# Performance work log

Hardware: AMD Instinct MI355X
Metric: run time of the kernel (lower is better)

## Reference

```python
import jax, jax.numpy as jnp
import numpy as np

IN_F = 4096
OUT_F = 4096
RANK = 16
N_BITS = 4
ALPHA = 1.0
GROUP = 128
Q_N = -(2 ** (N_BITS - 1))       # -8 for 4-bit signed
Q_P = 2 ** (N_BITS - 1) - 1      # +7
EPS = 1e-9


def setup_inputs() -> dict:
    key = jax.random.key(0)
    k0, k1, k2, k3, k4, k5 = jax.random.split(key, 6)
    x = jax.random.normal(k0, (8, 1024, IN_F), dtype=jnp.float32)
    w0 = jax.random.normal(k1, (OUT_F, IN_F), dtype=jnp.float32) * 0.02
    lora_a = jax.random.normal(k2, (RANK, IN_F), dtype=jnp.float32) * 0.02
    lora_b = jax.random.normal(k3, (OUT_F, RANK), dtype=jnp.float32) * 0.02
    num_groups = (OUT_F * IN_F) // GROUP
    q_scale = jnp.abs(jax.random.normal(k4, (num_groups,), dtype=jnp.float32)) * 0.01 + 0.005
    bias = jax.random.normal(k5, (OUT_F,), dtype=jnp.float32) * 0.01
    return {"x": x, "w0": w0, "lora_a": lora_a, "lora_b": lora_b,
            "q_scale": q_scale, "bias": bias}


def _quantize_weight(w0, lora_a, lora_b, q_scale):
    # LoRA merge: w_comb = w0 + alpha * (B @ A)   -> (OUT_F, IN_F)
    w_comb = w0 + ALPHA * (lora_b @ lora_a)
    num_groups = w_comb.size // GROUP
    w_g = w_comb.reshape(num_groups, GROUP)          # grouped view
    s = q_scale[:, None]                             # (G, 1) per-group scale
    w_scaled = w_g / (s + EPS)
    clamped = jnp.clip(w_scaled, Q_N, Q_P)
    q_int = jnp.round(clamped)
    w_q = (q_int * s).reshape(w_comb.shape)          # dequantized fake-quant weight
    return w_q


def reference(x, w0, lora_a, lora_b, q_scale, bias):
    w_q = _quantize_weight(w0, lora_a, lora_b, q_scale)
    # F.linear(x, w_q) + bias : (B, S, IN) @ (IN, OUT)
    return jnp.einsum('bsi,oi->bso', x, w_q) + bias
```

## Files before the change

kernel.cpp:

```cpp
#include <hip/hip_runtime.h>
#include <hip/hip_bf16.h>
#include <stdint.h>
#include <stddef.h>

#define IN_F   4096
#define OUT_F  4096
#define RANK   16
#define GROUP  128
#define M_TOT  8192

#define BM     256
#define BN     256
#define BK     32
#define NIT    (IN_F / BK)
#define HALF_B 16384
#define TILE_B 32768
#define LDS_B  (3 * TILE_B)

typedef __bf16 bf16_t;
typedef __bf16 bf16x4 __attribute__((ext_vector_type(4)));
typedef __bf16 bf16x8 __attribute__((ext_vector_type(8)));
typedef float  f32x4  __attribute__((ext_vector_type(4)));

__device__ static inline void load_lds16(const void* g, void* l) {
  __builtin_amdgcn_global_load_lds(
      (const __attribute__((address_space(1))) unsigned int*)g,
      (__attribute__((address_space(3))) unsigned int*)l,
      16, 0, 0);
}

__global__ void __launch_bounds__(256)
quant_kernel(const float* __restrict__ w0, const float* __restrict__ la,
             const float* __restrict__ lb, const float* __restrict__ qs,
             bf16_t* __restrict__ wq)
{
  const int o = blockIdx.y;
  const int i = blockIdx.x * 1024 + threadIdx.x * 4;

  __shared__ float lbr[RANK];
  if (threadIdx.x < RANK) lbr[threadIdx.x] = lb[o * RANK + threadIdx.x];
  __syncthreads();

  const size_t off = (size_t)o * IN_F + i;
  const float4 w = *(const float4*)(w0 + off);
  float a0 = w.x, a1 = w.y, a2 = w.z, a3 = w.w;
  #pragma unroll
  for (int r = 0; r < RANK; ++r) {
    const float4 av = *(const float4*)(la + (size_t)r * IN_F + i);
    const float bv = lbr[r];
    a0 = fmaf(bv, av.x, a0);
    a1 = fmaf(bv, av.y, a1);
    a2 = fmaf(bv, av.z, a2);
    a3 = fmaf(bv, av.w, a3);
  }
  const float s   = qs[o * (IN_F / GROUP) + (i >> 7)];
  const float inv = 1.0f / (s + 1e-9f);
  const float q0 = rintf(fminf(fmaxf(a0 * inv, -8.0f), 7.0f)) * s;
  const float q1 = rintf(fminf(fmaxf(a1 * inv, -8.0f), 7.0f)) * s;
  const float q2 = rintf(fminf(fmaxf(a2 * inv, -8.0f), 7.0f)) * s;
  const float q3 = rintf(fminf(fmaxf(a3 * inv, -8.0f), 7.0f)) * s;
  bf16x4 v;
  v[0] = (bf16_t)q0; v[1] = (bf16_t)q1; v[2] = (bf16_t)q2; v[3] = (bf16_t)q3;
  *(bf16x4*)(wq + off) = v;
}

__global__ void __launch_bounds__(256)
castx_kernel(const float* __restrict__ x, bf16_t* __restrict__ xb)
{
  const size_t i = ((size_t)blockIdx.x * 256 + threadIdx.x) * 8;
  const float4 a = *(const float4*)(x + i);
  const float4 b = *(const float4*)(x + i + 4);
  bf16x8 v;
  v[0] = (bf16_t)a.x; v[1] = (bf16_t)a.y; v[2] = (bf16_t)a.z; v[3] = (bf16_t)a.w;
  v[4] = (bf16_t)b.x; v[5] = (bf16_t)b.y; v[6] = (bf16_t)b.z; v[7] = (bf16_t)b.w;
  *(bf16x8*)(xb + i) = v;
}

__global__ void __launch_bounds__(512, 2)
gemm_kernel(const bf16_t* __restrict__ A, const bf16_t* __restrict__ Bw,
            const float* __restrict__ bias, float* __restrict__ C)
{
  extern __shared__ __align__(16) char smem[];

  const int tid  = threadIdx.x;
  const int lane = tid & 63;
  const int lr   = lane & 15;
  const int quad = lane >> 4;
  const int wid  = tid >> 6;
  const int wm   = wid >> 2;
  const int wn   = wid & 3;

  const int bid = blockIdx.x;
  const int swz = (bid & 7) * 64 + (bid >> 3);
  const int m0  = (swz >> 4) * BM;
  const int n0  = (swz & 15) * BN;

  const int srow = tid >> 2;
  const int scol = ((tid & 3) ^ ((tid >> 3) & 3)) * 8;
  const bf16_t* gA0 = A  + (size_t)(m0 + srow) * IN_F + scol;
  const bf16_t* gA1 = gA0 + (size_t)128 * IN_F;
  const bf16_t* gB0 = Bw + (size_t)(n0 + srow) * IN_F + scol;
  const bf16_t* gB1 = gB0 + (size_t)128 * IN_F;

  const int rswz = (quad ^ ((lr >> 1) & 3)) * 16;
  const int aOff = (wm * 128 + lr) * 64 + rswz;
  const int bOff = (wn * 64  + lr) * 64 + rswz;

  f32x4 acc[8][4];
  #pragma unroll
  for (int i = 0; i < 8; ++i)
    #pragma unroll
    for (int j = 0; j < 4; ++j)
      acc[i][j] = (f32x4){0.f, 0.f, 0.f, 0.f};

  bf16x8 bfr0[4], bfr1[4], afA[4], afB[4];

  auto stageA = [&](int T, char* buf) {
    const size_t ko = (size_t)T * BK;
    load_lds16(gA0 + ko, buf + tid * 16);
    load_lds16(gA1 + ko, buf + tid * 16 + 8192);
  };
  auto stageB = [&](int T, char* buf) {
    const size_t ko = (size_t)T * BK;
    load_lds16(gB0 + ko, buf + HALF_B + tid * 16);
    load_lds16(gB1 + ko, buf + HALF_B + tid * 16 + 8192);
  };

  auto ph_even = [&](int T, const char* rbuf, char* wbuf, bf16x8 (&bcur)[4]) {
    __builtin_amdgcn_s_barrier();
    __builtin_amdgcn_sched_barrier(0);
    if (T + 2 < NIT) stageA(T + 2, wbuf);
    #pragma unroll
    for (int f = 0; f < 4; ++f)
      afB[f] = *(const bf16x8*)(rbuf + aOff + 4096 + f * 1024);
    __builtin_amdgcn_sched_barrier(0);
    __builtin_amdgcn_s_setprio(1);
    #pragma unroll
    for (int fm = 0; fm < 4; ++fm)
      #pragma unroll
      for (int fn = 0; fn < 4; ++fn)
        acc[fm][fn] = __builtin_amdgcn_mfma_f32_16x16x32_bf16(
            afA[fm], bcur[fn], acc[fm][fn], 0, 0, 0);
    __builtin_amdgcn_s_setprio(0);
  };

  auto ph_odd = [&](int T, const char* rnext, char* wbuf,
                    bf16x8 (&bcur)[4], bf16x8 (&bnxt)[4]) {
    if (T + 2 < NIT) asm volatile("s_waitcnt vmcnt(2)" ::: "memory");
    else             asm volatile("s_waitcnt vmcnt(0)" ::: "memory");
    __builtin_amdgcn_s_barrier();
    __builtin_amdgcn_sched_barrier(0);
    if (T + 2 < NIT) stageB(T + 2, wbuf);
    if (T + 1 < NIT) {
      #pragma unroll
      for (int f = 0; f < 4; ++f)
        bnxt[f] = *(const bf16x8*)(rnext + HALF_B + bOff + f * 1024);
      #pragma unroll
      for (int f = 0; f < 4; ++f)
        afA[f] = *(const bf16x8*)(rnext + aOff + f * 1024);
    }
    __builtin_amdgcn_sched_barrier(0);
    __builtin_amdgcn_s_setprio(1);
    #pragma unroll
    for (int fm = 0; fm < 4; ++fm)
      #pragma unroll
      for (int fn = 0; fn < 4; ++fn)
        acc[4 + fm][fn] = __builtin_amdgcn_mfma_f32_16x16x32_bf16(
            afB[fm], bcur[fn], acc[4 + fm][fn], 0, 0, 0);
    __builtin_amdgcn_s_setprio(0);
  };

  {
    stageA(0, smem);          stageB(0, smem);
    stageA(1, smem + TILE_B); stageB(1, smem + TILE_B);
    asm volatile("s_waitcnt vmcnt(4)" ::: "memory");
    __builtin_amdgcn_s_barrier();
    __builtin_amdgcn_sched_barrier(0);
    #pragma unroll
    for (int f = 0; f < 4; ++f)
      bfr0[f] = *(const bf16x8*)(smem + HALF_B + bOff + f * 1024);
    #pragma unroll
    for (int f = 0; f < 4; ++f)
      afA[f] = *(const bf16x8*)(smem + aOff + f * 1024);
  }

  int rb = 0;
  for (int tt = 0; tt < NIT; tt += 2) {
    const int rb1 = (rb + 1 == 3) ? 0 : rb + 1;
    const int rb2 = (rb1 + 1 == 3) ? 0 : rb1 + 1;
    char* b_rb  = smem + rb  * TILE_B;
    char* b_rb1 = smem + rb1 * TILE_B;
    char* b_rb2 = smem + rb2 * TILE_B;

    ph_even(tt,     b_rb,  b_rb2, bfr0);
    ph_odd (tt,     b_rb1, b_rb2, bfr0, bfr1);
    ph_even(tt + 1, b_rb1, b_rb,  bfr1);
    ph_odd (tt + 1, b_rb2, b_rb,  bfr1, bfr0);

    rb = rb2;
  }

  #pragma unroll
  for (int fn = 0; fn < 4; ++fn) {
    const int gn = n0 + wn * 64 + fn * 16 + lr;
    const float bv = bias[gn];
    #pragma unroll
    for (int fm = 0; fm < 8; ++fm) {
      const int gm = m0 + wm * 128 + fm * 16 + quad * 4;
      #pragma unroll
      for (int r = 0; r < 4; ++r)
        C[(size_t)(gm + r) * OUT_F + gn] = acc[fm][fn][r] + bv;
    }
  }
}

extern "C" void kernel_launch(void* const* d_in, const int* in_sizes, int n_in,
                              void* d_out, int out_size, void* d_ws, size_t ws_size,
                              hipStream_t stream) {
  const float* x    = (const float*)d_in[0];
  const float* w0   = (const float*)d_in[1];
  const float* la   = (const float*)d_in[2];
  const float* lb   = (const float*)d_in[3];
  const float* qs   = (const float*)d_in[4];
  const float* bias = (const float*)d_in[5];
  float* out = (float*)d_out;

  bf16_t* wq = (bf16_t*)d_ws;
  bf16_t* xb = (bf16_t*)((char*)d_ws + (size_t)OUT_F * IN_F * 2);

  static bool attr_done = false;
  if (!attr_done) {
    (void)hipFuncSetAttribute((const void*)gemm_kernel,
                              hipFuncAttributeMaxDynamicSharedMemorySize,
                              LDS_B);
    attr_done = true;
  }

  quant_kernel<<<dim3(IN_F / 1024, OUT_F), 256, 0, stream>>>(w0, la, lb, qs, wq);
  castx_kernel<<<(M_TOT * IN_F) / (256 * 8), 256, 0, stream>>>(x, xb);
  gemm_kernel<<<dim3((M_TOT / BM) * (OUT_F / BN)), 512, LDS_B, stream>>>(
      xb, wq, bias, out);
}
```

Measured before the change: 544.2 us.

## Merge global-to-LDS stages into one barrier phase and interleave with MFMAs

Removes the barrier and the A-tile stage from the even phase. Both A and B next-tile loads are now issued in the odd phase after a full vmcnt(0) wait, so each K-step has one barrier instead of two. sched_group_barrier hints interleave the MFMAs with the LDS reads and VMEM issues, aiming to hide latency under matrix work. The trade-off is that waiting on all outstanding loads before the barrier shortens prefetch distance and may expose global memory latency.

New measurement: 560.2 us. 1.03x slower.

```diff
diff --git a/kernel.cpp b/kernel.cpp
--- a/kernel.cpp
+++ b/kernel.cpp
@@ -126,31 +126,34 @@
     load_lds16(gB1 + ko, buf + HALF_B + tid * 16 + 8192);
   };
 
-  auto ph_even = [&](int T, const char* rbuf, char* wbuf, bf16x8 (&bcur)[4]) {
-    __builtin_amdgcn_s_barrier();
-    __builtin_amdgcn_sched_barrier(0);
-    if (T + 2 < NIT) stageA(T + 2, wbuf);
+  auto ph_even = [&](int T, const char* rbuf, bf16x8 (&bcur)[4]) {
+    __builtin_amdgcn_s_setprio(1);
     #pragma unroll
     for (int f = 0; f < 4; ++f)
       afB[f] = *(const bf16x8*)(rbuf + aOff + 4096 + f * 1024);
-    __builtin_amdgcn_sched_barrier(0);
-    __builtin_amdgcn_s_setprio(1);
     #pragma unroll
     for (int fm = 0; fm < 4; ++fm)
       #pragma unroll
       for (int fn = 0; fn < 4; ++fn)
         acc[fm][fn] = __builtin_amdgcn_mfma_f32_16x16x32_bf16(
             afA[fm], bcur[fn], acc[fm][fn], 0, 0, 0);
+    #pragma unroll
+    for (int g = 0; g < 4; ++g) {
+      __builtin_amdgcn_sched_group_barrier(0x008, 2, 0);
+      __builtin_amdgcn_sched_group_barrier(0x100, 1, 0);
+    }
+    __builtin_amdgcn_sched_group_barrier(0x008, 8, 0);
     __builtin_amdgcn_s_setprio(0);
+    __builtin_amdgcn_sched_barrier(0);
   };
 
   auto ph_odd = [&](int T, const char* rnext, char* wbuf,
                     bf16x8 (&bcur)[4], bf16x8 (&bnxt)[4]) {
-    if (T + 2 < NIT) asm volatile("s_waitcnt vmcnt(2)" ::: "memory");
-    else             asm volatile("s_waitcnt vmcnt(0)" ::: "memory");
+    asm volatile("s_waitcnt vmcnt(0)" ::: "memory");
     __builtin_amdgcn_s_barrier();
     __builtin_amdgcn_sched_barrier(0);
-    if (T + 2 < NIT) stageB(T + 2, wbuf);
+    __builtin_amdgcn_s_setprio(1);
+    if (T + 2 < NIT) { stageA(T + 2, wbuf); stageB(T + 2, wbuf); }
     if (T + 1 < NIT) {
       #pragma unroll
       for (int f = 0; f < 4; ++f)
@@ -159,15 +162,25 @@
       for (int f = 0; f < 4; ++f)
         afA[f] = *(const bf16x8*)(rnext + aOff + f * 1024);
     }
-    __builtin_amdgcn_sched_barrier(0);
-    __builtin_amdgcn_s_setprio(1);
     #pragma unroll
     for (int fm = 0; fm < 4; ++fm)
       #pragma unroll
       for (int fn = 0; fn < 4; ++fn)
         acc[4 + fm][fn] = __builtin_amdgcn_mfma_f32_16x16x32_bf16(
             afB[fm], bcur[fn], acc[4 + fm][fn], 0, 0, 0);
+    #pragma unroll
+    for (int g = 0; g < 4; ++g) {
+      __builtin_amdgcn_sched_group_barrier(0x008, 1, 0);
+      __builtin_amdgcn_sched_group_barrier(0x010, 1, 0);
+    }
+    #pragma unroll
+    for (int g = 0; g < 8; ++g) {
+      __builtin_amdgcn_sched_group_barrier(0x008, 1, 0);
+      __builtin_amdgcn_sched_group_barrier(0x100, 1, 0);
+    }
+    __builtin_amdgcn_sched_group_barrier(0x008, 4, 0);
     __builtin_amdgcn_s_setprio(0);
+    __builtin_amdgcn_sched_barrier(0);
   };
 
   {
@@ -192,9 +205,9 @@
     char* b_rb1 = smem + rb1 * TILE_B;
     char* b_rb2 = smem + rb2 * TILE_B;
 
-    ph_even(tt,     b_rb,  b_rb2, bfr0);
+    ph_even(tt,     b_rb,  bfr0);
     ph_odd (tt,     b_rb1, b_rb2, bfr0, bfr1);
-    ph_even(tt + 1, b_rb1, b_rb,  bfr1);
+    ph_even(tt + 1, b_rb1, bfr1);
     ph_odd (tt + 1, b_rb2, b_rb,  bfr1, bfr0);
 
     rb = rb2;
```
